# Optimization experiments

Hardware: AMD Instinct MI355X
Metric: run time of the kernel (lower is better)

Reference implementation:

```python
import jax, jax.numpy as jnp
import numpy as np

H = 4        # no_heads
C = 32       # c_hidden per head
CQ = 128     # c_q = c_k = c_v
N = 256      # pair dim / seq len
B = 1


def setup_inputs() -> dict:
    key = jax.random.key(0)
    ks = jax.random.split(key, 8)
    q_x = jax.random.normal(ks[0], (B, N, N, CQ), dtype=jnp.float32)
    kv_x = jax.random.normal(ks[1], (B, N, N, CQ), dtype=jnp.float32)
    mask_bias = jnp.zeros((B, N, 1, 1, N), dtype=jnp.float32)
    pair_bias = jax.random.normal(ks[2], (B, 1, H, N, N), dtype=jnp.float32)
    s = 1.0 / np.sqrt(CQ)
    w_q = jax.random.normal(ks[3], (H * C, CQ), dtype=jnp.float32) * s
    w_k = jax.random.normal(ks[4], (H * C, CQ), dtype=jnp.float32) * s
    w_v = jax.random.normal(ks[5], (H * C, CQ), dtype=jnp.float32) * s
    w_g = jax.random.normal(ks[6], (H * C, CQ), dtype=jnp.float32) * s
    w_o = jax.random.normal(ks[7], (CQ, H * C), dtype=jnp.float32) * s
    return {"q_x": q_x, "kv_x": kv_x, "mask_bias": mask_bias,
            "pair_bias": pair_bias, "w_q": w_q, "w_k": w_k, "w_v": w_v,
            "w_g": w_g, "w_o": w_o}


def reference(q_x, kv_x, mask_bias, pair_bias, w_q, w_k, w_v, w_g, w_o):
    # project: [B, N, Q, c] -> [B, N, H, Q, C]
    def proj(x, w):
        y = jnp.einsum('...qc,dc->...qd', x, w)            # [B,N,Q,H*C]
        y = y.reshape(*y.shape[:-1], H, C)                 # [B,N,Q,H,C]
        return jnp.swapaxes(y, -2, -3)                     # [B,N,H,Q,C]

    q = proj(q_x, w_q) / jnp.sqrt(jnp.asarray(C, q_x.dtype))
    k = proj(kv_x, w_k)
    v = proj(kv_x, w_v)

    # scores [B, N, H, Q, K] with both biases added pre-softmax
    a = jnp.einsum('...hqd,...hkd->...hqk', q, k) + mask_bias + pair_bias
    a = jax.nn.softmax(a, axis=-1)
    o = jnp.einsum('...hqk,...hkd->...hqd', a, v)          # [B,N,H,Q,C]
    o = jnp.swapaxes(o, -2, -3)                            # [B,N,Q,H,C]
    o = o.reshape(*o.shape[:-2], H * C)                    # [B,N,Q,H*C]

    g = jax.nn.sigmoid(jnp.einsum('...qc,dc->...qd', q_x, w_g))
    o = o * g
    return jnp.einsum('...qd,cd->...qc', o, w_o)           # [B,N,Q,c_q]
```

## Files before the change

kernel.cpp:

```cpp
#include <hip/hip_runtime.h>
#include <hip/hip_bf16.h>

#define H 4
#define C 32
#define CQ 128
#define NSEQ 256
#define HC 128

typedef __bf16 bf16;
typedef __bf16 bf16x8 __attribute__((ext_vector_type(8)));
typedef __bf16 bf16x4 __attribute__((ext_vector_type(4)));
typedef float f32x4 __attribute__((ext_vector_type(4)));

#define MFMA16(a, b, c) __builtin_amdgcn_mfma_f32_16x16x32_bf16(a, b, c, 0, 0, 0)

#define LOG2E 1.4426950408889634f

__device__ __forceinline__ bf16x8 cvt8(float4 a, float4 b) {
    return (bf16x8){(bf16)a.x, (bf16)a.y, (bf16)a.z, (bf16)a.w,
                    (bf16)b.x, (bf16)b.y, (bf16)b.z, (bf16)b.w};
}

__global__ __launch_bounds__(256) void prep_weights(const float* __restrict__ wq,
                                                    const float* __restrict__ wk,
                                                    const float* __restrict__ wv,
                                                    const float* __restrict__ wg,
                                                    const float* __restrict__ wo,
                                                    bf16* __restrict__ dst) {
    const int m = blockIdx.y;
    const float* src = (m == 0) ? wq : (m == 1) ? wk : (m == 2) ? wv : (m == 3) ? wg : wo;
    int i = blockIdx.x * 256 + threadIdx.x;
    float4 v = ((const float4*)src)[i];
    bf16x4 b = {(bf16)v.x, (bf16)v.y, (bf16)v.z, (bf16)v.w};
    ((bf16x4*)(dst + (size_t)m * 16384))[i] = b;
}

__global__ __launch_bounds__(512) void proj_all(const float* __restrict__ qx,
                                                const float* __restrict__ kvx,
                                                const bf16* __restrict__ wbf,
                                                bf16* __restrict__ qo,
                                                bf16* __restrict__ go,
                                                bf16* __restrict__ ko,
                                                bf16* __restrict__ vo) {
    __shared__ bf16 w1s[128][136];
    __shared__ bf16 w2s[128][136];
    __shared__ bf16 xs[2][64][136];

    const int t = threadIdx.x;
    const int mode = blockIdx.y;

    const float* x = mode ? kvx : qx;
    const bf16* w1 = wbf + (mode ? 1 : 0) * 16384;
    const bf16* w2 = wbf + (mode ? 2 : 3) * 16384;
    bf16* o1 = mode ? ko : qo;
    bf16* o2 = mode ? vo : go;

    const int row_blk = blockIdx.x * 256;
    const int sr = t >> 3, sc = (t & 7) * 16;

    #pragma unroll
    for (int i = t; i < 2048; i += 512) {
        int row = i >> 4, col = (i & 15) * 8;
        *(bf16x8*)&w1s[row][col] = *(const bf16x8*)&w1[row * CQ + col];
        *(bf16x8*)&w2s[row][col] = *(const bf16x8*)&w2[row * CQ + col];
    }
    {
        const float* p = x + (size_t)(row_blk + sr) * CQ + sc;
        float4 v0 = *(const float4*)p, v1 = *(const float4*)(p + 4);
        float4 v2 = *(const float4*)(p + 8), v3 = *(const float4*)(p + 12);
        *(bf16x8*)&xs[0][sr][sc] = cvt8(v0, v1);
        *(bf16x8*)&xs[0][sr][sc + 8] = cvt8(v2, v3);
    }
    __syncthreads();

    const int w = t >> 6, l = t & 63, lr = l & 15, lg = l >> 4;

    bf16x8 a1[4], a2[4];
    #pragma unroll
    for (int ks = 0; ks < 4; ks++) {
        a1[ks] = *(const bf16x8*)&w1s[w * 16 + lr][ks * 32 + lg * 8];
        a2[ks] = *(const bf16x8*)&w2s[w * 16 + lr][ks * 32 + lg * 8];
    }

    const float qscale = 0.17677669529663687f * LOG2E;

    #pragma unroll 1
    for (int it = 0; it < 4; it++) {
        const int cur = it & 1;

        float4 n0, n1, n2, n3;
        if (it < 3) {
            const float* p = x + (size_t)(row_blk + (it + 1) * 64 + sr) * CQ + sc;
            n0 = *(const float4*)p;
            n1 = *(const float4*)(p + 4);
            n2 = *(const float4*)(p + 8);
            n3 = *(const float4*)(p + 12);
        }

        #pragma unroll
        for (int rt = 0; rt < 4; rt++) {
            bf16x8 b[4];
            #pragma unroll
            for (int ks = 0; ks < 4; ks++)
                b[ks] = *(const bf16x8*)&xs[cur][rt * 16 + lr][ks * 32 + lg * 8];

            f32x4 acc1 = (f32x4)0.f, acc2 = (f32x4)0.f;
            #pragma unroll
            for (int ks = 0; ks < 4; ks++) {
                acc1 = MFMA16(a1[ks], b[ks], acc1);
                acc2 = MFMA16(a2[ks], b[ks], acc2);
            }

            bf16x4 st1, st2;
            #pragma unroll
            for (int r = 0; r < 4; r++) {
                float v1 = acc1[r], v2 = acc2[r];
                if (mode == 0) {
                    v1 *= qscale;
                    v2 = __builtin_amdgcn_rcpf(1.f + __builtin_amdgcn_exp2f(-v2 * LOG2E));
                }
                st1[r] = (bf16)v1;
                st2[r] = (bf16)v2;
            }
            const size_t obase =
                (size_t)(row_blk + it * 64 + rt * 16 + lr) * HC + w * 16 + lg * 4;
            *(bf16x4*)&o1[obase] = st1;
            *(bf16x4*)&o2[obase] = st2;
        }

        if (it < 3) {
            *(bf16x8*)&xs[cur ^ 1][sr][sc] = cvt8(n0, n1);
            *(bf16x8*)&xs[cur ^ 1][sr][sc + 8] = cvt8(n2, n3);
        }
        __syncthreads();
    }
}

__global__ __launch_bounds__(256) void attn_kernel(const bf16* __restrict__ qw,
                                                   const bf16* __restrict__ kw,
                                                   const bf16* __restrict__ vw,
                                                   const bf16* __restrict__ gw,
                                                   const float* __restrict__ pair_bias,
                                                   const float* __restrict__ mask_bias,
                                                   bf16* __restrict__ ow) {
    const int wg = blockIdx.x;
    const int swz = ((wg & 7) << 9) + (wg >> 3);
    const int qc = swz & 3;
    const int n1 = (swz >> 2) & 255;
    const int h = swz >> 10;

    __shared__ bf16 klds[256][40];
    __shared__ bf16 vts[32][256];
    __shared__ bf16 ps[4][16][132];

    const int t = threadIdx.x;

    {
        const size_t base = ((size_t)n1 * NSEQ) * HC + (size_t)h * C;
        const int rr = t >> 2, cc4 = t & 3, ch = cc4 * 8;
        #pragma unroll
        for (int p = 0; p < 4; p++) {
            int row = p * 64 + rr;
            bf16x8 kv = *(const bf16x8*)&kw[base + (size_t)row * HC + ch];
            *(bf16x8*)&klds[row][ch] = kv;
            bf16x8 vv = *(const bf16x8*)&vw[base + (size_t)row * HC + ch];
            #pragma unroll
            for (int j = 0; j < 8; j++) {
                int colw = row ^ (cc4 << 4) ^ (j << 3);
                vts[ch + j][colw] = vv[j];
            }
        }
    }

    const int w = t >> 6, l = t & 63, lr = l & 15, lg = l >> 4;
    const int qbase = qc * 64 + w * 16;

    bf16x8 qf = *(const bf16x8*)&qw[((size_t)(n1 * NSEQ + qbase + lr)) * HC + h * C + lg * 8];

    const float* pb = pair_bias + (size_t)h * NSEQ * NSEQ;
    const float* mb = mask_bias + (size_t)n1 * NSEQ;

    __syncthreads();

    f32x4 s[16];
    #pragma unroll
    for (int kt = 0; kt < 16; kt++) {
        float mbk = mb[kt * 16 + lr] * LOG2E;
        #pragma unroll
        for (int r = 0; r < 4; r++)
            s[kt][r] = fmaf(pb[(size_t)(qbase + lg * 4 + r) * NSEQ + kt * 16 + lr],
                            LOG2E, mbk);
    }
    #pragma unroll
    for (int kt = 0; kt < 16; kt++) {
        bf16x8 kf = *(const bf16x8*)&klds[kt * 16 + lr][lg * 8];
        s[kt] = MFMA16(qf, kf, s[kt]);
    }

    float pinv[4];
    #pragma unroll
    for (int r = 0; r < 4; r++) {
        float mx = s[0][r];
        #pragma unroll
        for (int kt = 1; kt < 16; kt++) mx = fmaxf(mx, s[kt][r]);
        #pragma unroll
        for (int msk = 8; msk >= 1; msk >>= 1) mx = fmaxf(mx, __shfl_xor(mx, msk, 64));
        float sum = 0.f;
        #pragma unroll
        for (int kt = 0; kt < 16; kt++) {
            float e = __builtin_amdgcn_exp2f(s[kt][r] - mx);
            s[kt][r] = e;
            sum += e;
        }
        #pragma unroll
        for (int msk = 8; msk >= 1; msk >>= 1) sum += __shfl_xor(sum, msk, 64);
        pinv[r] = __builtin_amdgcn_rcpf(sum);
    }

    f32x4 o[2];
    o[0] = (f32x4)0.f;
    o[1] = (f32x4)0.f;
    #pragma unroll
    for (int hf = 0; hf < 2; hf++) {
        #pragma unroll
        for (int kt2 = 0; kt2 < 8; kt2++) {
            #pragma unroll
            for (int r = 0; r < 4; r++)
                ps[w][lg * 4 + r][kt2 * 16 + lr] = (bf16)(s[hf * 8 + kt2][r] * pinv[r]);
        }
        #pragma unroll
        for (int kh = 0; kh < 4; kh++) {
            bf16x8 pf = *(const bf16x8*)&ps[w][lr][kh * 32 + lg * 8];
            #pragma unroll
            for (int ct = 0; ct < 2; ct++) {
                int g2 = (2 * ct + (lr >> 3)) & 3;
                int col0 = (hf * 128 + kh * 32 + lg * 8) ^ (g2 << 4) ^ ((lr & 7) << 3);
                bf16x8 vf = *(const bf16x8*)&vts[ct * 16 + lr][col0];
                o[ct] = MFMA16(pf, vf, o[ct]);
            }
        }
    }

    #pragma unroll
    for (int ct = 0; ct < 2; ct++) {
        #pragma unroll
        for (int r = 0; r < 4; r++) {
            size_t idx = ((size_t)(n1 * NSEQ + qbase + lg * 4 + r)) * HC + (size_t)h * C +
                         ct * 16 + lr;
            float gv = (float)gw[idx];
            ow[idx] = (bf16)(o[ct][r] * gv);
        }
    }
}

__global__ __launch_bounds__(512) void out_proj(const bf16* __restrict__ og,
                                                const bf16* __restrict__ wo,
                                                float* __restrict__ out) {
    __shared__ bf16 ws[128][136];
    __shared__ bf16 xs[2][64][136];

    const int t = threadIdx.x;
    const int row_blk = blockIdx.x * 256;
    const int sr = t >> 3, sc = (t & 7) * 16;

    #pragma unroll
    for (int i = t; i < 2048; i += 512) {
        int row = i >> 4, col = (i & 15) * 8;
        *(bf16x8*)&ws[row][col] = *(const bf16x8*)&wo[row * CQ + col];
    }
    {
        const bf16* p = og + (size_t)(row_blk + sr) * HC + sc;
        *(bf16x8*)&xs[0][sr][sc] = *(const bf16x8*)p;
        *(bf16x8*)&xs[0][sr][sc + 8] = *(const bf16x8*)(p + 8);
    }
    __syncthreads();

    const int w = t >> 6, l = t & 63, lr = l & 15, lg = l >> 4;

    bf16x8 a[4];
    #pragma unroll
    for (int ks = 0; ks < 4; ks++)
        a[ks] = *(const bf16x8*)&ws[w * 16 + lr][ks * 32 + lg * 8];

    #pragma unroll 1
    for (int it = 0; it < 4; it++) {
        const int cur = it & 1;

        bf16x8 m0, m1;
        if (it < 3) {
            const bf16* p = og + (size_t)(row_blk + (it + 1) * 64 + sr) * HC + sc;
            m0 = *(const bf16x8*)p;
            m1 = *(const bf16x8*)(p + 8);
        }

        #pragma unroll
        for (int rt = 0; rt < 4; rt++) {
            bf16x8 b[4];
            #pragma unroll
            for (int ks = 0; ks < 4; ks++)
                b[ks] = *(const bf16x8*)&xs[cur][rt * 16 + lr][ks * 32 + lg * 8];

            f32x4 acc = (f32x4)0.f;
            #pragma unroll
            for (int ks = 0; ks < 4; ks++)
                acc = MFMA16(a[ks], b[ks], acc);

            *(float4*)&out[(size_t)(row_blk + it * 64 + rt * 16 + lr) * CQ + w * 16 + lg * 4] =
                (float4){acc[0], acc[1], acc[2], acc[3]};
        }

        if (it < 3) {
            *(bf16x8*)&xs[cur ^ 1][sr][sc] = m0;
            *(bf16x8*)&xs[cur ^ 1][sr][sc + 8] = m1;
        }
        __syncthreads();
    }
}

extern "C" void kernel_launch(void* const* d_in, const int* in_sizes, int n_in,
                              void* d_out, int out_size, void* d_ws, size_t ws_size,
                              hipStream_t stream) {
    const float* q_x = (const float*)d_in[0];
    const float* kv_x = (const float*)d_in[1];
    const float* mask_bias = (const float*)d_in[2];
    const float* pair_bias = (const float*)d_in[3];
    const float* w_q = (const float*)d_in[4];
    const float* w_k = (const float*)d_in[5];
    const float* w_v = (const float*)d_in[6];
    const float* w_g = (const float*)d_in[7];
    const float* w_o = (const float*)d_in[8];

    const size_t M = (size_t)NSEQ * NSEQ;
    bf16* wbf = (bf16*)d_ws;
    bf16* qws = wbf + 5 * 16384;
    bf16* gws = qws + M * HC;
    bf16* kws = gws + M * HC;
    bf16* vws = kws + M * HC;
    bf16* ows = vws + M * HC;

    prep_weights<<<dim3(16, 5), 256, 0, stream>>>(w_q, w_k, w_v, w_g, w_o, wbf);
    proj_all<<<dim3(256, 2), 512, 0, stream>>>(q_x, kv_x, wbf, qws, gws, kws, vws);
    attn_kernel<<<dim3(4096), 256, 0, stream>>>(qws, kws, vws, gws, pair_bias,
                                                mask_bias, ows);
    out_proj<<<dim3(256), 512, 0, stream>>>(ows, wbf + 4 * 16384, (float*)d_out);
}
```

Baseline: 87.17 us.

## Fuse output projection into attention kernel, looping over heads per block

Each attention block now handles all four heads for its 64 query rows, looping over heads and keeping the gated per-head outputs in registers (staged through LDS). The output projection with w_o is then done directly by MFMA in the same kernel, writing the final fp32 output. This removes the intermediate bf16 gated-attention buffer round trip and the separate out_proj launch. In exchange the grid shrinks from 4096 to 1024 blocks, each doing serial per-head work with extra barriers, and w_o is read from global memory per wave instead of from LDS.

```diff
diff --git a/kernel.cpp b/kernel.cpp
--- a/kernel.cpp
+++ b/kernel.cpp
@@ -136,184 +136,149 @@
     }
 }
 
-__global__ __launch_bounds__(256) void attn_kernel(const bf16* __restrict__ qw,
-                                                   const bf16* __restrict__ kw,
-                                                   const bf16* __restrict__ vw,
-                                                   const bf16* __restrict__ gw,
-                                                   const float* __restrict__ pair_bias,
-                                                   const float* __restrict__ mask_bias,
-                                                   bf16* __restrict__ ow) {
+__global__ __launch_bounds__(256) void attn_fused(const bf16* __restrict__ qw,
+                                                  const bf16* __restrict__ kw,
+                                                  const bf16* __restrict__ vw,
+                                                  const bf16* __restrict__ gw,
+                                                  const bf16* __restrict__ wo,
+                                                  const float* __restrict__ pair_bias,
+                                                  const float* __restrict__ mask_bias,
+                                                  float* __restrict__ out) {
     const int wg = blockIdx.x;
-    const int swz = ((wg & 7) << 9) + (wg >> 3);
+    const int swz = ((wg & 7) << 7) + (wg >> 3);
     const int qc = swz & 3;
-    const int n1 = (swz >> 2) & 255;
-    const int h = swz >> 10;
+    const int n1 = swz >> 2;
 
     __shared__ bf16 klds[256][40];
     __shared__ bf16 vts[32][256];
     __shared__ bf16 ps[4][16][132];
 
     const int t = threadIdx.x;
-
-    {
-        const size_t base = ((size_t)n1 * NSEQ) * HC + (size_t)h * C;
-        const int rr = t >> 2, cc4 = t & 3, ch = cc4 * 8;
-        #pragma unroll
-        for (int p = 0; p < 4; p++) {
-            int row = p * 64 + rr;
-            bf16x8 kv = *(const bf16x8*)&kw[base + (size_t)row * HC + ch];
-            *(bf16x8*)&klds[row][ch] = kv;
-            bf16x8 vv = *(const bf16x8*)&vw[base + (size_t)row * HC + ch];
-            #pragma unroll
-            for (int j = 0; j < 8; j++) {
-                int colw = row ^ (cc4 << 4) ^ (j << 3);
-                vts[ch + j][colw] = vv[j];
-            }
-        }
-    }
-
     const int w = t >> 6, l = t & 63, lr = l & 15, lg = l >> 4;
     const int qbase = qc * 64 + w * 16;
-
-    bf16x8 qf = *(const bf16x8*)&qw[((size_t)(n1 * NSEQ + qbase + lr)) * HC + h * C + lg * 8];
-
-    const float* pb = pair_bias + (size_t)h * NSEQ * NSEQ;
-    const float* mb = mask_bias + (size_t)n1 * NSEQ;
-
-    __syncthreads();
-
-    f32x4 s[16];
+    const int rr = t >> 2, cc4 = t & 3, ch = cc4 * 8;
+
+    float mbr[16];
+    {
+        const float* mb = mask_bias + (size_t)n1 * NSEQ;
+        #pragma unroll
+        for (int kt = 0; kt < 16; kt++) mbr[kt] = mb[kt * 16 + lr] * LOG2E;
+    }
+
+    bf16x8 og[4];
+
     #pragma unroll
-    for (int kt = 0; kt < 16; kt++) {
-        float mbk = mb[kt * 16 + lr] * LOG2E;
-        #pragma unroll
-        for (int r = 0; r < 4; r++)
-            s[kt][r] = fmaf(pb[(size_t)(qbase + lg * 4 + r) * NSEQ + kt * 16 + lr],
-                            LOG2E, mbk);
-    }
+    for (int h = 0; h < 4; h++) {
+        if (h > 0) __syncthreads();
+
+        {
+            const size_t base = ((size_t)n1 * NSEQ) * HC + (size_t)h * C;
+            #pragma unroll
+            for (int p = 0; p < 4; p++) {
+                int row = p * 64 + rr;
+                bf16x8 kv = *(const bf16x8*)&kw[base + (size_t)row * HC + ch];
+                *(bf16x8*)&klds[row][ch] = kv;
+                bf16x8 vv = *(const bf16x8*)&vw[base + (size_t)row * HC + ch];
+                #pragma unroll
+                for (int j = 0; j < 8; j++) {
+                    int colw = row ^ (cc4 << 4) ^ (j << 3);
+                    vts[ch + j][colw] = vv[j];
+                }
+            }
+        }
+
+        bf16x8 qf =
+            *(const bf16x8*)&qw[((size_t)(n1 * NSEQ + qbase + lr)) * HC + h * C + lg * 8];
+
+        const float* pb = pair_bias + (size_t)h * NSEQ * NSEQ;
+        f32x4 s[16];
+        #pragma unroll
+        for (int kt = 0; kt < 16; kt++) {
+            #pragma unroll
+            for (int r = 0; r < 4; r++)
+                s[kt][r] = fmaf(pb[(size_t)(qbase + lg * 4 + r) * NSEQ + kt * 16 + lr],
+                                LOG2E, mbr[kt]);
+        }
+
+        __syncthreads();
+
+        #pragma unroll
+        for (int kt = 0; kt < 16; kt++) {
+            bf16x8 kf = *(const bf16x8*)&klds[kt * 16 + lr][lg * 8];
+            s[kt] = MFMA16(qf, kf, s[kt]);
+        }
+
+        float pinv[4];
+        #pragma unroll
+        for (int r = 0; r < 4; r++) {
+            float mx = s[0][r];
+            #pragma unroll
+            for (int kt = 1; kt < 16; kt++) mx = fmaxf(mx, s[kt][r]);
+            #pragma unroll
+            for (int msk = 8; msk >= 1; msk >>= 1) mx = fmaxf(mx, __shfl_xor(mx, msk, 64));
+            float sum = 0.f;
+            #pragma unroll
+            for (int kt = 0; kt < 16; kt++) {
+                float e = __builtin_amdgcn_exp2f(s[kt][r] - mx);
+                s[kt][r] = e;
+                sum += e;
+            }
+            #pragma unroll
+            for (int msk = 8; msk >= 1; msk >>= 1) sum += __shfl_xor(sum, msk, 64);
+            pinv[r] = __builtin_amdgcn_rcpf(sum);
+        }
+
+        f32x4 o[2];
+        o[0] = (f32x4)0.f;
+        o[1] = (f32x4)0.f;
+        #pragma unroll
+        for (int hf = 0; hf < 2; hf++) {
+            #pragma unroll
+            for (int kt2 = 0; kt2 < 8; kt2++) {
+                #pragma unroll
+                for (int r = 0; r < 4; r++)
+                    ps[w][lg * 4 + r][kt2 * 16 + lr] = (bf16)(s[hf * 8 + kt2][r] * pinv[r]);
+            }
+            #pragma unroll
+            for (int kh = 0; kh < 4; kh++) {
+                bf16x8 pf = *(const bf16x8*)&ps[w][lr][kh * 32 + lg * 8];
+                #pragma unroll
+                for (int ct = 0; ct < 2; ct++) {
+                    int g2 = (2 * ct + (lr >> 3)) & 3;
+                    int col0 = (hf * 128 + kh * 32 + lg * 8) ^ (g2 << 4) ^ ((lr & 7) << 3);
+                    bf16x8 vf = *(const bf16x8*)&vts[ct * 16 + lr][col0];
+                    o[ct] = MFMA16(pf, vf, o[ct]);
+                }
+            }
+        }
+
+        #pragma unroll
+        for (int ct = 0; ct < 2; ct++) {
+            #pragma unroll
+            for (int r = 0; r < 4; r++) {
+                size_t gidx = ((size_t)(n1 * NSEQ + qbase + lg * 4 + r)) * HC +
+                              (size_t)h * C + ct * 16 + lr;
+                float gv = (float)gw[gidx];
+                ps[w][lg * 4 + r][ct * 16 + lr] = (bf16)(o[ct][r] * gv);
+            }
+        }
+        og[h] = *(const bf16x8*)&ps[w][lr][lg * 8];
+    }
+
     #pragma unroll
-    for (int kt = 0; kt < 16; kt++) {
-        bf16x8 kf = *(const bf16x8*)&klds[kt * 16 + lr][lg * 8];
-        s[kt] = MFMA16(qf, kf, s[kt]);
-    }
-
-    float pinv[4];
-    #pragma unroll
-    for (int r = 0; r < 4; r++) {
-        float mx = s[0][r];
-        #pragma unroll
-        for (int kt = 1; kt < 16; kt++) mx = fmaxf(mx, s[kt][r]);
-        #pragma unroll
-        for (int msk = 8; msk >= 1; msk >>= 1) mx = fmaxf(mx, __shfl_xor(mx, msk, 64));
-        float sum = 0.f;
-        #pragma unroll
-        for (int kt = 0; kt < 16; kt++) {
-            float e = __builtin_amdgcn_exp2f(s[kt][r] - mx);
-            s[kt][r] = e;
-            sum += e;
-        }
-        #pragma unroll
-        for (int msk = 8; msk >= 1; msk >>= 1) sum += __shfl_xor(sum, msk, 64);
-        pinv[r] = __builtin_amdgcn_rcpf(sum);
-    }
-
-    f32x4 o[2];
-    o[0] = (f32x4)0.f;
-    o[1] = (f32x4)0.f;
-    #pragma unroll
-    for (int hf = 0; hf < 2; hf++) {
-        #pragma unroll
-        for (int kt2 = 0; kt2 < 8; kt2++) {
-            #pragma unroll
-            for (int r = 0; r < 4; r++)
-                ps[w][lg * 4 + r][kt2 * 16 + lr] = (bf16)(s[hf * 8 + kt2][r] * pinv[r]);
-        }
-        #pragma unroll
-        for (int kh = 0; kh < 4; kh++) {
-            bf16x8 pf = *(const bf16x8*)&ps[w][lr][kh * 32 + lg * 8];
-            #pragma unroll
-            for (int ct = 0; ct < 2; ct++) {
-                int g2 = (2 * ct + (lr >> 3)) & 3;
-                int col0 = (hf * 128 + kh * 32 + lg * 8) ^ (g2 << 4) ^ ((lr & 7) << 3);
-                bf16x8 vf = *(const bf16x8*)&vts[ct * 16 + lr][col0];
-                o[ct] = MFMA16(pf, vf, o[ct]);
-            }
-        }
-    }
-
-    #pragma unroll
-    for (int ct = 0; ct < 2; ct++) {
-        #pragma unroll
-        for (int r = 0; r < 4; r++) {
-            size_t idx = ((size_t)(n1 * NSEQ + qbase + lg * 4 + r)) * HC + (size_t)h * C +
-                         ct * 16 + lr;
-            float gv = (float)gw[idx];
-            ow[idx] = (bf16)(o[ct][r] * gv);
-        }
-    }
-}
-
-__global__ __launch_bounds__(512) void out_proj(const bf16* __restrict__ og,
-                                                const bf16* __restrict__ wo,
-                                                float* __restrict__ out) {
-    __shared__ bf16 ws[128][136];
-    __shared__ bf16 xs[2][64][136];
-
-    const int t = threadIdx.x;
-    const int row_blk = blockIdx.x * 256;
-    const int sr = t >> 3, sc = (t & 7) * 16;
-
-    #pragma unroll
-    for (int i = t; i < 2048; i += 512) {
-        int row = i >> 4, col = (i & 15) * 8;
-        *(bf16x8*)&ws[row][col] = *(const bf16x8*)&wo[row * CQ + col];
-    }
-    {
-        const bf16* p = og + (size_t)(row_blk + sr) * HC + sc;
-        *(bf16x8*)&xs[0][sr][sc] = *(const bf16x8*)p;
-        *(bf16x8*)&xs[0][sr][sc + 8] = *(const bf16x8*)(p + 8);
-    }
-    __syncthreads();
-
-    const int w = t >> 6, l = t & 63, lr = l & 15, lg = l >> 4;
-
-    bf16x8 a[4];
-    #pragma unroll
-    for (int ks = 0; ks < 4; ks++)
-        a[ks] = *(const bf16x8*)&ws[w * 16 + lr][ks * 32 + lg * 8];
-
-    #pragma unroll 1
-    for (int it = 0; it < 4; it++) {
-        const int cur = it & 1;
-
-        bf16x8 m0, m1;
-        if (it < 3) {
-            const bf16* p = og + (size_t)(row_blk + (it + 1) * 64 + sr) * HC + sc;
-            m0 = *(const bf16x8*)p;
-            m1 = *(const bf16x8*)(p + 8);
-        }
-
-        #pragma unroll
-        for (int rt = 0; rt < 4; rt++) {
-            bf16x8 b[4];
-            #pragma unroll
-            for (int ks = 0; ks < 4; ks++)
-                b[ks] = *(const bf16x8*)&xs[cur][rt * 16 + lr][ks * 32 + lg * 8];
-
-            f32x4 acc = (f32x4)0.f;
-            #pragma unroll
-            for (int ks = 0; ks < 4; ks++)
-                acc = MFMA16(a[ks], b[ks], acc);
-
-            *(float4*)&out[(size_t)(row_blk + it * 64 + rt * 16 + lr) * CQ + w * 16 + lg * 4] =
-                (float4){acc[0], acc[1], acc[2], acc[3]};
-        }
-
-        if (it < 3) {
-            *(bf16x8*)&xs[cur ^ 1][sr][sc] = m0;
-            *(bf16x8*)&xs[cur ^ 1][sr][sc + 8] = m1;
-        }
-        __syncthreads();
+    for (int nt = 0; nt < 8; nt++) {
+        bf16x8 a[4];
+        #pragma unroll
+        for (int ks = 0; ks < 4; ks++)
+            a[ks] = *(const bf16x8*)&wo[(size_t)(nt * 16 + lr) * CQ + ks * 32 + lg * 8];
+
+        f32x4 acc = (f32x4)0.f;
+        #pragma unroll
+        for (int ks = 0; ks < 4; ks++)
+            acc = MFMA16(a[ks], og[ks], acc);
+
+        *(float4*)&out[(size_t)(n1 * NSEQ + qbase + lr) * CQ + nt * 16 + lg * 4] =
+            (float4){acc[0], acc[1], acc[2], acc[3]};
     }
 }
 
@@ -336,11 +301,9 @@
     bf16* gws = qws + M * HC;
     bf16* kws = gws + M * HC;
     bf16* vws = kws + M * HC;
-    bf16* ows = vws + M * HC;
 
     prep_weights<<<dim3(16, 5), 256, 0, stream>>>(w_q, w_k, w_v, w_g, w_o, wbf);
     proj_all<<<dim3(256, 2), 512, 0, stream>>>(q_x, kv_x, wbf, qws, gws, kws, vws);
-    attn_kernel<<<dim3(4096), 256, 0, stream>>>(qws, kws, vws, gws, pair_bias,
-                                                mask_bias, ows);
-    out_proj<<<dim3(256), 512, 0, stream>>>(ows, wbf + 4 * 16384, (float*)d_out);
-}
+    attn_fused<<<dim3(1024), 256, 0, stream>>>(qws, kws, vws, gws, wbf + 4 * 16384,
+                                               pair_bias, mask_bias, (float*)d_out);
+}
```

Measured after the change: 149.6 us. 1.72x slower.
